# Kernel optimization log

Measured on AMD Instinct MI355X. Metric: run time of the kernel, lower is better.

Reference implementation:

```python
import jax, jax.numpy as jnp
import numpy as np

N = 100000   # nodes
E = 400000   # edges
G = 5000     # graphs (20 nodes each)
H = 128      # hidden_channels
ATOM_D, BOND_D, BOOL_D = 16, 8, 2
NODE_D = 30 + ATOM_D + 3 * BOOL_D   # 52
EDGE_D = 2 + BOND_D + 3 * BOOL_D    # 16


def setup_inputs() -> dict:
    key = jax.random.key(0)
    ks = jax.random.split(key, 24)
    rn = lambda k, shape: jax.random.normal(k, shape, dtype=jnp.float32) * 0.05
    # node features: [atom_idx, 10 continuous, 3 bools]
    atom_idx = jax.random.randint(ks[0], (N,), 1, 119)
    node_cont = jax.random.normal(ks[1], (N, 10), dtype=jnp.float32)
    node_bool = jax.random.randint(ks[2], (N, 3), 0, 2)
    x = jnp.concatenate([atom_idx[:, None].astype(jnp.float32), node_cont,
                         node_bool.astype(jnp.float32)], axis=1)
    # edge features: [bond_idx, 1 continuous, 3 bools]
    bond_idx = jax.random.randint(ks[3], (E,), 1, 22)
    edge_cont = jax.random.normal(ks[4], (E, 1), dtype=jnp.float32)
    edge_bool = jax.random.randint(ks[5], (E, 3), 0, 2)
    edge_attr = jnp.concatenate([bond_idx[:, None].astype(jnp.float32), edge_cont,
                                 edge_bool.astype(jnp.float32)], axis=1)
    edge_index = jax.random.randint(ks[6], (2, E), 0, N)
    batch = jnp.repeat(jnp.arange(G, dtype=jnp.int32), N // G)
    # embeddings (with padding rows zeroed, as nn.Embedding padding_idx)
    atom_emb = rn(ks[7], (119, ATOM_D)).at[0].set(0.0)
    bond_emb = rn(ks[8], (22, BOND_D)).at[0].set(0.0)
    bool_emb = rn(ks[9], (3, BOOL_D)).at[2].set(0.0)
    Wn = rn(ks[10], (10, 30)); bn = jnp.zeros((30,), jnp.float32)
    We = rn(ks[11], (1, 2));   be = jnp.zeros((2,), jnp.float32)
    Wl1 = rn(ks[12], (NODE_D, H)); bl1 = jnp.zeros((H,), jnp.float32)
    Wr1 = rn(ks[13], (NODE_D, H)); br1 = jnp.zeros((H,), jnp.float32)
    Wedge1 = rn(ks[14], (EDGE_D, H)); att1 = rn(ks[15], (H,))
    bias1 = jnp.zeros((H,), jnp.float32)
    Wl2 = rn(ks[16], (H, H)); bl2 = jnp.zeros((H,), jnp.float32)
    Wr2 = rn(ks[17], (H, H)); br2 = jnp.zeros((H,), jnp.float32)
    Wedge2 = rn(ks[18], (EDGE_D, H)); att2 = rn(ks[19], (H,))
    bias2 = jnp.zeros((H,), jnp.float32)
    return dict(x=x, edge_index=edge_index, edge_attr=edge_attr, batch=batch,
                atom_emb=atom_emb, bond_emb=bond_emb, bool_emb=bool_emb,
                Wn=Wn, bn=bn, We=We, be=be,
                Wl1=Wl1, bl1=bl1, Wr1=Wr1, br1=br1, Wedge1=Wedge1, att1=att1, bias1=bias1,
                Wl2=Wl2, bl2=bl2, Wr2=Wr2, br2=br2, Wedge2=Wedge2, att2=att2, bias2=bias2)


def _gatv2(h, src, dst, e_lin, Wl, bl, Wr, br, att, bias):
    # PyG GATv2Conv, heads=1: xl = lin_l(x) (source), xr = lin_r(x) (target)
    xl = h @ Wl + bl
    xr = h @ Wr + br
    m = xl[src] + xr[dst] + e_lin                      # [E', H]
    a = jax.nn.leaky_relu(m, 0.2) @ att                # [E']
    amax = jax.ops.segment_max(a, dst, num_segments=N)
    ex = jnp.exp(a - amax[dst])
    denom = jax.ops.segment_sum(ex, dst, num_segments=N)
    alpha = ex / denom[dst]                            # softmax over incoming edges
    out = jax.ops.segment_sum(alpha[:, None] * xl[src], dst, num_segments=N)
    return out + bias


def reference(x, edge_index, edge_attr, batch,
              atom_emb, bond_emb, bool_emb, Wn, bn, We, be,
              Wl1, bl1, Wr1, br1, Wedge1, att1, bias1,
              Wl2, bl2, Wr2, br2, Wedge2, att2, bias2):
    # --- encode nodes ---
    ai = x[:, 0].astype(jnp.int32)
    nb = x[:, 11:14].astype(jnp.int32)
    h = jnp.concatenate([atom_emb[ai], x[:, 1:11] @ Wn + bn,
                         bool_emb[nb[:, 0]], bool_emb[nb[:, 1]], bool_emb[nb[:, 2]]], axis=1)
    # --- encode edges ---
    bi = edge_attr[:, 0].astype(jnp.int32)
    eb = edge_attr[:, 2:5].astype(jnp.int32)
    e = jnp.concatenate([bond_emb[bi], edge_attr[:, 1:2] @ We + be,
                         bool_emb[eb[:, 0]], bool_emb[eb[:, 1]], bool_emb[eb[:, 2]]], axis=1)
    src, dst = edge_index[0], edge_index[1]
    # --- add self loops with fill_value='mean' (mean of in-edge attrs per node) ---
    cnt = jax.ops.segment_sum(jnp.ones((E,), h.dtype), dst, num_segments=N)
    loop_attr = jax.ops.segment_sum(e, dst, num_segments=N) / jnp.maximum(cnt, 1.0)[:, None]
    e_full = jnp.concatenate([e, loop_attr], axis=0)          # [E+N, EDGE_D]
    loop = jnp.arange(N, dtype=src.dtype)
    src_f = jnp.concatenate([src, loop])
    dst_f = jnp.concatenate([dst, loop])
    # --- 3 GATv2 layers (layers 2 and 3 share weights, as in the original) ---
    h = jax.nn.relu(_gatv2(h, src_f, dst_f, e_full @ Wedge1, Wl1, bl1, Wr1, br1, att1, bias1))
    e_lin2 = e_full @ Wedge2
    h = jax.nn.relu(_gatv2(h, src_f, dst_f, e_lin2, Wl2, bl2, Wr2, br2, att2, bias2))
    h = jax.nn.relu(_gatv2(h, src_f, dst_f, e_lin2, Wl2, bl2, Wr2, br2, att2, bias2))
    # --- global_max_pool readout ---
    return jax.ops.segment_max(h, batch, num_segments=G)
```

## Files before the change

### kernel.cpp

```cpp
#include <hip/hip_runtime.h>
#include <hip/hip_fp16.h>

#define N_NODES 100000
#define N_EDGES 400000
#define N_GRAPHS 5000
#define NPG 20
#define SCAN_NB 256
#define SCAN_CHUNK ((N_NODES + SCAN_NB - 1) / SCAN_NB)
#define TAB_STRIDE (256 * 128 + 128)
#define F1 8192
#define F2 16384
#define NB_ENC ((N_NODES + 255) / 256)
#define NB_HIST ((N_EDGES + 255) / 256)

typedef __attribute__((ext_vector_type(8))) _Float16 f16x8;
typedef __attribute__((ext_vector_type(2))) _Float16 h2;
typedef __attribute__((ext_vector_type(4))) float f32x4;

#define DPP_QUAD_XOR1 0xB1
#define DPP_QUAD_XOR2 0x4E
#define DPP_ROW_HALF_MIRROR 0x141
#define DPP_ROW_MIRROR 0x140
template <int CTRL>
__device__ __forceinline__ float dpp_add(float x) {
  int p = __builtin_amdgcn_update_dpp(0, __float_as_int(x), CTRL, 0xf, 0xf, true);
  return x + __int_as_float(p);
}

__global__ __launch_bounds__(256) void k_prologue(
    const float* __restrict__ x, const float* __restrict__ atom_emb,
    const float* __restrict__ bool_emb, const float* __restrict__ Wn,
    const float* __restrict__ bn, __half* __restrict__ h0,
    const int* __restrict__ dst, int* __restrict__ cnt,
    const float* __restrict__ Wedge1, const float* __restrict__ Wedge2,
    const float* __restrict__ bond_emb, const float* __restrict__ We,
    const float* __restrict__ be, __half* __restrict__ tabs,
    const float* __restrict__ Wl1, const float* __restrict__ Wr1,
    const float* __restrict__ Wl2, const float* __restrict__ Wr2,
    unsigned short* __restrict__ fr) {
  int b = blockIdx.x, tid = threadIdx.x;
  if (b < NB_ENC) {
    int n = b * 256 + tid;
    if (n >= N_NODES) return;
    const float* xr = x + (size_t)n * 14;
    int ai = (int)xr[0];
    _Float16 hr[64];
    #pragma unroll
    for (int j = 0; j < 16; j++) hr[j] = (_Float16)atom_emb[ai * 16 + j];
    float xc[10];
    #pragma unroll
    for (int k = 0; k < 10; k++) xc[k] = xr[1 + k];
    #pragma unroll
    for (int c = 0; c < 30; c++) {
      float s = bn[c];
      #pragma unroll
      for (int k = 0; k < 10; k++) s += xc[k] * Wn[k * 30 + c];
      hr[16 + c] = (_Float16)s;
    }
    #pragma unroll
    for (int t = 0; t < 3; t++) {
      int bb = (int)xr[11 + t];
      hr[46 + 2 * t]     = (_Float16)bool_emb[2 * bb];
      hr[46 + 2 * t + 1] = (_Float16)bool_emb[2 * bb + 1];
    }
    #pragma unroll
    for (int j = 52; j < 64; j++) hr[j] = (_Float16)0.0f;
    uint4* d4 = (uint4*)(h0 + (size_t)n * 64);
    const uint4* s4 = (const uint4*)hr;
    #pragma unroll
    for (int j = 0; j < 8; j++) d4[j] = s4[j];
  } else if (b < NB_ENC + NB_HIST) {
    int e = (b - NB_ENC) * 256 + tid;
    if (e >= N_EDGES) return;
    atomicAdd(cnt + dst[e], 1);
  } else if (b == NB_ENC + NB_HIST) {
    int s = tid >> 7, c = tid & 127;
    const float* W = s ? Wedge2 : Wedge1;
    __half* T12 = tabs + (size_t)s * TAB_STRIDE;
    __half* v   = T12 + 256 * 128;
    float w8 = W[8 * 128 + c], w9 = W[9 * 128 + c];
    v[c] = __float2half(We[0] * w8 + We[1] * w9);
    float cst = be[0] * w8 + be[1] * w9;
    float bond[22];
    for (int bb = 0; bb < 22; bb++) {
      float acc = 0.f;
      #pragma unroll
      for (int k = 0; k < 8; k++) acc += bond_emb[bb * 8 + k] * W[k * 128 + c];
      bond[bb] = acc;
    }
    for (int combo = 0; combo < 8; combo++) {
      float t2 = cst;
      #pragma unroll
      for (int tt = 0; tt < 3; tt++) {
        int bt = (combo >> tt) & 1;
        t2 += bool_emb[bt * 2 + 0] * W[(10 + 2 * tt + 0) * 128 + c];
        t2 += bool_emb[bt * 2 + 1] * W[(10 + 2 * tt + 1) * 128 + c];
      }
      for (int bb = 0; bb < 22; bb++)
        T12[(combo * 32 + bb) * 128 + c] = __float2half(bond[bb] + t2);
      for (int bb = 22; bb < 32; bb++)
        T12[(combo * 32 + bb) * 128 + c] = __float2half(0.f);
    }
  } else {
    int g = (b - (NB_ENC + NB_HIST + 1)) * 256 + tid;
    const float* W; int K; unsigned short* base; int fl;
    if (g < 1024)      { W = Wl1; K = 52;  base = fr;               fl = g; }
    else if (g < 2048) { W = Wr1; K = 52;  base = fr + F1;          fl = g - 1024; }
    else if (g < 4096) { W = Wl2; K = 128; base = fr + 2 * F1;      fl = g - 2048; }
    else if (g < 6144) { W = Wr2; K = 128; base = fr + 2 * F1 + F2; fl = g - 4096; }
    else return;
    int l = fl & 63, ctn = fl >> 6;
    int tn = ctn & 7, c = ctn >> 3;
    int n = tn * 16 + (l & 15);
    int kb = c * 32 + (l >> 4) * 8;
    unsigned h8[8];
    #pragma unroll
    for (int j = 0; j < 8; j++) {
      int k = kb + j;
      float v = (k < K) ? W[(size_t)k * 128 + n] : 0.f;
      __half hv = __float2half(v);
      h8[j] = (unsigned)*(unsigned short*)&hv;
    }
    uint4 hv4 = make_uint4(h8[0] | (h8[1] << 16), h8[2] | (h8[3] << 16),
                           h8[4] | (h8[5] << 16), h8[6] | (h8[7] << 16));
    *(uint4*)(base + (size_t)fl * 8) = hv4;
  }
}

__global__ __launch_bounds__(256) void k_scan1(const int* __restrict__ cnt,
                                               int* __restrict__ bsum,
                                               int* __restrict__ ghist) {
  __shared__ int red[256];
  __shared__ int lh[64];
  int b = blockIdx.x, t = threadIdx.x;
  if (t < 64) lh[t] = 0;
  __syncthreads();
  int beg = b * SCAN_CHUNK;
  int end = beg + SCAN_CHUNK; if (end > N_NODES) end = N_NODES;
  int s = 0;
  for (int i = beg + t; i < end; i += 256) {
    int cv = cnt[i];
    s += cv + 1;
    atomicAdd(&lh[cv < 63 ? cv : 63], 1);
  }
  red[t] = s;
  __syncthreads();
  for (int off = 128; off > 0; off >>= 1) {
    if (t < off) red[t] += red[t + off];
    __syncthreads();
  }
  if (t == 0) bsum[b] = red[0];
  if (t < 64 && lh[t] > 0) atomicAdd(&ghist[t], lh[t]);
}

__global__ __launch_bounds__(256) void k_scan3(const int* __restrict__ cnt,
                                               const int* __restrict__ bsum,
                                               int* __restrict__ indptr,
                                               int* __restrict__ cursor,
                                               const int* __restrict__ ghist,
                                               int* __restrict__ gcur) {
  __shared__ int sh[256];
  __shared__ int carry;
  int b = blockIdx.x, t = threadIdx.x;
  sh[t] = bsum[t];
  __syncthreads();
  for (int off = 1; off < 256; off <<= 1) {
    int v = (t >= off) ? sh[t - off] : 0;
    __syncthreads();
    sh[t] += v;
    __syncthreads();
  }
  if (t == 0) carry = (b > 0) ? sh[b - 1] : 0;
  __syncthreads();
  int beg = b * SCAN_CHUNK;
  int end = beg + SCAN_CHUNK; if (end > N_NODES) end = N_NODES;
  for (int base = beg; base < end; base += 256) {
    int i = base + t;
    int v = (i < end) ? cnt[i] + 1 : 0;
    sh[t] = v;
    __syncthreads();
    for (int off = 1; off < 256; off <<= 1) {
      int u = (t >= off) ? sh[t - off] : 0;
      __syncthreads();
      sh[t] += u;
      __syncthreads();
    }
    int excl = sh[t] - v;
    if (i < end) {
      int val = carry + excl;
      indptr[i] = val;
      cursor[i] = val;
    }
    __syncthreads();
    if (t == 255) carry += sh[255];
    __syncthreads();
  }
  if (b == 0 && t == 0) indptr[N_NODES] = N_EDGES + N_NODES;
  if (b == 0) {
    __syncthreads();
    if (t < 64) sh[t] = ghist[t];
    __syncthreads();
    if (t == 0) {
      int run = 0;
      for (int i = 0; i < 64; i++) { int v = sh[i]; sh[i] = run; run += v; }
    }
    __syncthreads();
    if (t < 64) gcur[t] = sh[t];
  }
}

__global__ void k_fill(const int* __restrict__ srcA,
                       const int* __restrict__ dst,
                       const float* __restrict__ eattr,
                       int* __restrict__ cursor,
                       int4* __restrict__ scode,
                       const int* __restrict__ cnt,
                       int* __restrict__ gcur,
                       int* __restrict__ perm) {
  int b = blockIdx.x, t = threadIdx.x;
  if (b < NB_HIST) {
    int e = b * 256 + t;
    if (e >= N_EDGES) return;
    const float* r = eattr + (size_t)e * 5;
    int bi = (int)r[0];
    float ec = r[1];
    int combo = (int)r[2] + 2 * (int)r[3] + 4 * (int)r[4];
    int meta = bi | (combo << 5);
    int d = dst[e];
    int p = atomicAdd(&cursor[d], 1);
    scode[p] = make_int4(srcA[e], meta, __float_as_int(ec), 0);
  } else {
    __shared__ int lh[64];
    __shared__ int lbase[64];
    if (t < 64) lh[t] = 0;
    __syncthreads();
    int n = (b - NB_HIST) * 256 + t;
    bool v = (n < N_NODES);
    int dc = 0, r = 0;
    if (v) {
      int cv = cnt[n];
      dc = cv < 63 ? cv : 63;
      r = atomicAdd(&lh[dc], 1);
    }
    __syncthreads();
    if (t < 64 && lh[t] > 0) lbase[t] = atomicAdd(&gcur[t], lh[t]);
    __syncthreads();
    if (v) perm[lbase[dc] + r] = n;
  }
}

template <int KPAD>
__global__ __launch_bounds__(256, 4) void k_gemm2m(const __half* __restrict__ A,
                                                   const unsigned short* __restrict__ WfL,
                                                   const unsigned short* __restrict__ WfR,
                                                   const float* __restrict__ bl_,
                                                   const float* __restrict__ br_,
                                                   __half* __restrict__ outl,
                                                   __half* __restrict__ outr) {
  __shared__ unsigned short Bs[2][8192];
  const int tid = threadIdx.x;
  const int wv = tid >> 6, lane = tid & 63;
  const int tw = blockIdx.x * 4 + wv;
  const bool active = (tw < N_NODES / 16);
  const int ml = lane & 15, q = lane >> 4;
  const int m0 = active ? tw * 16 : 0;
  f32x4 accL[8], accR[8];
  #pragma unroll
  for (int t = 0; t < 8; t++) {
    accL[t] = (f32x4){0.f, 0.f, 0.f, 0.f};
    accR[t] = (f32x4){0.f, 0.f, 0.f, 0.f};
  }
  const _Float16* ar0 = (const _Float16*)A + (size_t)(m0 + ml) * KPAD + q * 8;
  constexpr int NC2 = KPAD / 64;
  for (int c2 = 0; c2 < NC2; c2++) {
    #pragma unroll
    for (int i0 = 0; i0 < 1024; i0 += 256) {
      int i = i0 + tid;
      size_t g = ((size_t)c2 * 1024 + i) * 8;
      *(uint4*)(&Bs[0][i * 8]) = *(const uint4*)(WfL + g);
      *(uint4*)(&Bs[1][i * 8]) = *(const uint4*)(WfR + g);
    }
    __syncthreads();
    #pragma unroll
    for (int sub = 0; sub < 2; sub++) {
      f16x8 a = *(const f16x8*)(ar0 + c2 * 64 + sub * 32);
      #pragma unroll
      for (int t = 0; t < 8; t++) {
        int idx = (sub * 512 + t * 64 + lane) * 8;
        f16x8 bL = *(const f16x8*)(&Bs[0][idx]);
        f16x8 bR = *(const f16x8*)(&Bs[1][idx]);
        accL[t] = __builtin_amdgcn_mfma_f32_16x16x32_f16(a, bL, accL[t], 0, 0, 0);
        accR[t] = __builtin_amdgcn_mfma_f32_16x16x32_f16(a, bR, accR[t], 0, 0, 0);
      }
    }
    __syncthreads();
  }
  __syncthreads();
  if (!active) return;
  __half* eb = (__half*)&Bs[0][0] + wv * 2048;
  const int srow = q * 4;
  const int rrow0 = lane >> 4;
  const int rcol = (lane & 15) * 8;
  #pragma unroll
  for (int t = 0; t < 8; t++) {
    int n = t * 16 + ml;
    float bL = bl_[n];
    #pragma unroll
    for (int r = 0; r < 4; r++)
      eb[(srow + r) * 128 + n] = __float2half(accL[t][r] + bL);
  }
  #pragma unroll
  for (int pp = 0; pp < 4; pp++) {
    uint4 v = *(const uint4*)(eb + pp * 512 + lane * 8);
    *(uint4*)(outl + (size_t)(m0 + pp * 4 + rrow0) * 128 + rcol) = v;
  }
  #pragma unroll
  for (int t = 0; t < 8; t++) {
    int n = t * 16 + ml;
    float bR = br_[n];
    #pragma unroll
    for (int r = 0; r < 4; r++)
      eb[(srow + r) * 128 + n] = __float2half(accR[t][r] + bR);
  }
  #pragma unroll
  for (int pp = 0; pp < 4; pp++) {
    uint4 v = *(const uint4*)(eb + pp * 512 + lane * 8);
    *(uint4*)(outr + (size_t)(m0 + pp * 4 + rrow0) * 128 + rcol) = v;
  }
}

__global__ __launch_bounds__(256) void k_gat(const __half* __restrict__ xl,
                                             const __half* __restrict__ xr,
                                             const int* __restrict__ indptr,
                                             const int4* __restrict__ scode,
                                             const __half* __restrict__ tabs,
                                             const float* __restrict__ att,
                                             const float* __restrict__ bias,
                                             __half* __restrict__ hout,
                                             const int* __restrict__ perm) {
  int wid = (blockIdx.x * 256 + threadIdx.x) >> 6;
  int nw = (gridDim.x * 256) >> 6;
  int lane = threadIdx.x & 63;
  int q4 = lane >> 4;
  int c = (lane & 15) * 8;
  const __half* T12 = tabs;
  uint4 vu = *(const uint4*)(tabs + 256 * 128 + c);
  h2 v4[4] = {*reinterpret_cast<h2*>(&vu.x), *reinterpret_cast<h2*>(&vu.y),
              *reinterpret_cast<h2*>(&vu.z), *reinterpret_cast<h2*>(&vu.w)};
  float4 af0 = *(const float4*)(att + c);
  float4 af1 = *(const float4*)(att + c + 4);
  h2 a4[4] = {{(_Float16)af0.x, (_Float16)af0.y}, {(_Float16)af0.z, (_Float16)af0.w},
              {(_Float16)af1.x, (_Float16)af1.y}, {(_Float16)af1.z, (_Float16)af1.w}};
  float bb[8];
  {
    float4 b0 = *(const float4*)(bias + c);
    float4 b1 = *(const float4*)(bias + c + 4);
    bb[0] = b0.x; bb[1] = b0.y; bb[2] = b0.z; bb[3] = b0.w;
    bb[4] = b1.x; bb[5] = b1.y; bb[6] = b1.z; bb[7] = b1.w;
  }
  const h2 z2 = {(_Float16)0.f, (_Float16)0.f};
  const h2 k2 = {(_Float16)0.2f, (_Float16)0.2f};
  wid = __builtin_amdgcn_readfirstlane(wid);
  const int stride = nw * 4;
  int nb = wid * 4;
  if (nb >= N_NODES) return;
  int n = perm[nb + q4];
  int bg = indptr[n], en = indptr[n + 1];
  uint4 xru = *(const uint4*)(xr + (size_t)n * 128 + c);
  while (true) {
    int nb2 = nb + stride;
    bool has2 = (nb2 < N_NODES);
    int n2 = has2 ? perm[nb2 + q4] : n;
    int bg2 = indptr[n2];
    int en2 = indptr[n2 + 1];
    uint4 xru2 = *(const uint4*)(xr + (size_t)n2 * 128 + c);
    int beg = bg, end1 = en - 1;
    int last = (end1 > beg) ? end1 - 1 : beg;
    h2 xrv[4] = {*reinterpret_cast<h2*>(&xru.x), *reinterpret_cast<h2*>(&xru.y),
                 *reinterpret_cast<h2*>(&xru.z), *reinterpret_cast<h2*>(&xru.w)};
    float denom = 0.f;
    float acc[8] = {0.f, 0.f, 0.f, 0.f, 0.f, 0.f, 0.f, 0.f};
    h2 els[4] = {z2, z2, z2, z2};
    int my_it = (end1 - beg + 3) >> 2;
    int m1 = my_it, m2;
    m2 = __shfl_xor(m1, 16, 64); m1 = m1 > m2 ? m1 : m2;
    m2 = __shfl_xor(m1, 32, 64); m1 = m1 > m2 ? m1 : m2;
    int iters = m1;
    for (int it = 0; it < iters; it++) {
      int j = beg + it * 4;
      int4 sc4[4]; h2 xlv[4][4]; float tt[4];
      bool val[4];
      #pragma unroll
      for (int u = 0; u < 4; u++) {
        val[u] = (j + u < end1);
        int jj = val[u] ? j + u : last;
        sc4[u] = scode[jj];
      }
      #pragma unroll
      for (int u = 0; u < 4; u++) {
        int s = val[u] ? sc4[u].x : n;
        uint4 lv = *(const uint4*)(xl + (size_t)s * 128 + c);
        xlv[u][0] = *reinterpret_cast<h2*>(&lv.x);
        xlv[u][1] = *reinterpret_cast<h2*>(&lv.y);
        xlv[u][2] = *reinterpret_cast<h2*>(&lv.z);
        xlv[u][3] = *reinterpret_cast<h2*>(&lv.w);
      }
      #pragma unroll
      for (int u = 0; u < 4; u++) {
        int meta = val[u] ? (sc4[u].y & 255) : 255;
        float ec = val[u] ? __int_as_float(sc4[u].z) : 0.f;
        uint4 tv = *(const uint4*)(T12 + (size_t)meta * 128 + c);
        h2 t4[4] = {*reinterpret_cast<h2*>(&tv.x), *reinterpret_cast<h2*>(&tv.y),
                    *reinterpret_cast<h2*>(&tv.z), *reinterpret_cast<h2*>(&tv.w)};
        _Float16 eh = (_Float16)ec;
        h2 eh2 = {eh, eh};
        h2 d = z2;
        #pragma unroll
        for (int k = 0; k < 4; k++) {
          h2 el = eh2 * v4[k] + t4[k];
          h2 m = xlv[u][k] + xrv[k] + el;
          h2 l = __builtin_elementwise_max(m, z2) + k2 * __builtin_elementwise_min(m, z2);
          d += l * a4[k];
          els[k] += el;
        }
        tt[u] = (float)d[0] + (float)d[1];
      }
      #pragma unroll
      for (int u = 0; u < 4; u++) tt[u] = dpp_add<DPP_QUAD_XOR1>(tt[u]);
      #pragma unroll
      for (int u = 0; u < 4; u++) tt[u] = dpp_add<DPP_QUAD_XOR2>(tt[u]);
      #pragma unroll
      for (int u = 0; u < 4; u++) tt[u] = dpp_add<DPP_ROW_HALF_MIRROR>(tt[u]);
      #pragma unroll
      for (int u = 0; u < 4; u++) tt[u] = dpp_add<DPP_ROW_MIRROR>(tt[u]);
      #pragma unroll
      for (int u = 0; u < 4; u++) {
        float ex = val[u] ? __expf(tt[u]) : 0.f;
        denom += ex;
        #pragma unroll
        for (int k = 0; k < 4; k++) {
          acc[2 * k]     += ex * (float)xlv[u][k][0];
          acc[2 * k + 1] += ex * (float)xlv[u][k][1];
        }
      }
    }
    int cntn = end1 - beg;
    float inv_cnt = 1.0f / (float)(cntn > 0 ? cntn : 1);
    uint4 xnu = *(const uint4*)(xl + (size_t)n * 128 + c);
    h2 xn[4] = {*reinterpret_cast<h2*>(&xnu.x), *reinterpret_cast<h2*>(&xnu.y),
                *reinterpret_cast<h2*>(&xnu.z), *reinterpret_cast<h2*>(&xnu.w)};
    float afv[8] = {af0.x, af0.y, af0.z, af0.w, af1.x, af1.y, af1.z, af1.w};
    float ts = 0.f;
    float xnf[8];
    #pragma unroll
    for (int k = 0; k < 4; k++) {
      #pragma unroll
      for (int hh = 0; hh < 2; hh++) {
        int i = 2 * k + hh;
        xnf[i] = (float)xn[k][hh];
        float m = xnf[i] + (float)xrv[k][hh] + (float)els[k][hh] * inv_cnt;
        float l = m > 0.f ? m : 0.2f * m;
        ts += l * afv[i];
      }
    }
    ts = dpp_add<DPP_QUAD_XOR1>(ts);
    ts = dpp_add<DPP_QUAD_XOR2>(ts);
    ts = dpp_add<DPP_ROW_HALF_MIRROR>(ts);
    ts = dpp_add<DPP_ROW_MIRROR>(ts);
    float ex = __expf(ts);
    denom += ex;
    #pragma unroll
    for (int i = 0; i < 8; i++) acc[i] += ex * xnf[i];
    float invd = 1.0f / denom;
    h2 p[4];
    #pragma unroll
    for (int k = 0; k < 4; k++) {
      float o0 = acc[2 * k] * invd + bb[2 * k];
      float o1 = acc[2 * k + 1] * invd + bb[2 * k + 1];
      o0 = o0 > 0.f ? o0 : 0.f;
      o1 = o1 > 0.f ? o1 : 0.f;
      p[k] = (h2){(_Float16)o0, (_Float16)o1};
    }
    uint4 st = make_uint4(*reinterpret_cast<unsigned*>(&p[0]),
                          *reinterpret_cast<unsigned*>(&p[1]),
                          *reinterpret_cast<unsigned*>(&p[2]),
                          *reinterpret_cast<unsigned*>(&p[3]));
    *(uint4*)(hout + (size_t)n * 128 + c) = st;
    if (!has2) break;
    nb = nb2; n = n2; bg = bg2; en = en2; xru = xru2;
  }
}

__global__ void k_readout(const __half* __restrict__ h, float* __restrict__ out) {
  int wid = (blockIdx.x * blockDim.x + threadIdx.x) >> 6;
  int lane = threadIdx.x & 63;
  if (wid >= N_GRAPHS) return;
  int c = lane * 2;
  float m0 = -1e30f, m1 = -1e30f;
  for (int i = 0; i < NPG; i++) {
    unsigned v = *(const unsigned*)(h + ((size_t)(wid * NPG + i)) * 128 + c);
    h2 f = *reinterpret_cast<h2*>(&v);
    m0 = fmaxf(m0, (float)f[0]);
    m1 = fmaxf(m1, (float)f[1]);
  }
  float2 o; o.x = m0; o.y = m1;
  *(float2*)(out + (size_t)wid * 128 + c) = o;
}

extern "C" void kernel_launch(void* const* d_in, const int* in_sizes, int n_in,
                              void* d_out, int out_size, void* d_ws, size_t ws_size,
                              hipStream_t stream) {
  (void)in_sizes; (void)n_in; (void)out_size; (void)ws_size;
  const float* x        = (const float*)d_in[0];
  const int*   eindex   = (const int*)d_in[1];
  const float* eattr    = (const float*)d_in[2];
  const float* atom_emb = (const float*)d_in[4];
  const float* bond_emb = (const float*)d_in[5];
  const float* bool_emb = (const float*)d_in[6];
  const float* Wn   = (const float*)d_in[7];
  const float* bn   = (const float*)d_in[8];
  const float* We   = (const float*)d_in[9];
  const float* be   = (const float*)d_in[10];
  const float* Wl1  = (const float*)d_in[11];
  const float* bl1  = (const float*)d_in[12];
  const float* Wr1  = (const float*)d_in[13];
  const float* br1  = (const float*)d_in[14];
  const float* Wedge1 = (const float*)d_in[15];
  const float* att1 = (const float*)d_in[16];
  const float* bias1 = (const float*)d_in[17];
  const float* Wl2  = (const float*)d_in[18];
  const float* bl2  = (const float*)d_in[19];
  const float* Wr2  = (const float*)d_in[20];
  const float* br2  = (const float*)d_in[21];
  const float* Wedge2 = (const float*)d_in[22];
  const float* att2 = (const float*)d_in[23];
  const float* bias2 = (const float*)d_in[24];

  const int* srcA = eindex;
  const int* dstA = eindex + N_EDGES;

  char* p = (char*)d_ws;
  auto alloc = [&](size_t bytes) {
    char* r = p;
    p += (bytes + 255) & ~(size_t)255;
    return r;
  };
  __half* h0     = (__half*)alloc((size_t)N_NODES * 64 * 2);
  __half* h      = (__half*)alloc((size_t)N_NODES * 128 * 2);
  __half* xl     = (__half*)alloc((size_t)N_NODES * 128 * 2);
  __half* xrb    = (__half*)alloc((size_t)N_NODES * 128 * 2);
  int*    cnt    = (int*)alloc((size_t)N_NODES * 4);
  int*    indptr = (int*)alloc((size_t)(N_NODES + 1) * 4);
  int*    cursor = (int*)alloc((size_t)N_NODES * 4);
  int4*   scode  = (int4*)alloc((size_t)(N_EDGES + N_NODES) * 16);
  __half* tabs   = (__half*)alloc((size_t)2 * TAB_STRIDE * 2);
  unsigned short* wfrag = (unsigned short*)alloc((size_t)(2 * F1 + 2 * F2) * 2);
  int*    bsum   = (int*)alloc((size_t)SCAN_NB * 4);
  int*    ghist  = (int*)alloc((size_t)64 * 4);
  int*    gcur   = (int*)alloc((size_t)64 * 4);
  int*    perm   = (int*)alloc((size_t)N_NODES * 4);

  (void)hipMemsetAsync(cnt, 0, (size_t)N_NODES * 4, stream);
  (void)hipMemsetAsync(ghist, 0, (size_t)64 * 4, stream);

  k_prologue<<<NB_ENC + NB_HIST + 1 + 24, 256, 0, stream>>>(
      x, atom_emb, bool_emb, Wn, bn, h0, dstA, cnt,
      Wedge1, Wedge2, bond_emb, We, be, tabs,
      Wl1, Wr1, Wl2, Wr2, wfrag);
  k_scan1<<<SCAN_NB, 256, 0, stream>>>(cnt, bsum, ghist);
  k_scan3<<<SCAN_NB, 256, 0, stream>>>(cnt, bsum, indptr, cursor, ghist, gcur);
  k_fill<<<NB_HIST + NB_ENC, 256, 0, stream>>>(srcA, dstA, eattr, cursor, scode,
                                               cnt, gcur, perm);

  const unsigned short* f_l1 = wfrag;
  const unsigned short* f_r1 = wfrag + F1;
  const unsigned short* f_l2 = wfrag + 2 * F1;
  const unsigned short* f_r2 = wfrag + 2 * F1 + F2;

  const int GB2 = (N_NODES / 16 + 3) / 4;

  k_gemm2m<64><<<GB2, 256, 0, stream>>>(h0, f_l1, f_r1, bl1, br1, xl, xrb);
  k_gat<<<2048, 256, 0, stream>>>(xl, xrb, indptr, scode, tabs, att1, bias1, h, perm);

  k_gemm2m<128><<<GB2, 256, 0, stream>>>(h, f_l2, f_r2, bl2, br2, xl, xrb);
  k_gat<<<2048, 256, 0, stream>>>(xl, xrb, indptr, scode, tabs + TAB_STRIDE, att2, bias2, h, perm);

  k_gemm2m<128><<<GB2, 256, 0, stream>>>(h, f_l2, f_r2, bl2, br2, xl, xrb);
  k_gat<<<2048, 256, 0, stream>>>(xl, xrb, indptr, scode, tabs + TAB_STRIDE, att2, bias2, h, perm);

  k_readout<<<(N_GRAPHS * 64 + 255) / 256, 256, 0, stream>>>(h, (float*)d_out);
}
```

Baseline: 334.6 us.

## Software-pipeline GAT edge loop with double-buffered gathers and prefetched edge codes

Restructures the per-node edge aggregation loop in the GAT kernel into a two-stage software pipeline. Edge codes are loaded two iterations ahead, and the xl-row and table gathers for the next iteration are issued before the current iteration's compute, using A/B register buffers. The goal is to hide global-memory gather latency behind the attention math. The extra buffers raise VGPR pressure and may lower occupancy.

```diff
diff --git a/kernel.cpp b/kernel.cpp
--- a/kernel.cpp
+++ b/kernel.cpp
@@ -344,9 +344,9 @@
   int q4 = lane >> 4;
   int c = (lane & 15) * 8;
   const __half* T12 = tabs;
-  uint4 vu = *(const uint4*)(tabs + 256 * 128 + c);
-  h2 v4[4] = {*reinterpret_cast<h2*>(&vu.x), *reinterpret_cast<h2*>(&vu.y),
-              *reinterpret_cast<h2*>(&vu.z), *reinterpret_cast<h2*>(&vu.w)};
+  uint4 vu_ = *(const uint4*)(tabs + 256 * 128 + c);
+  h2 v4[4] = {*reinterpret_cast<h2*>(&vu_.x), *reinterpret_cast<h2*>(&vu_.y),
+              *reinterpret_cast<h2*>(&vu_.z), *reinterpret_cast<h2*>(&vu_.w)};
   float4 af0 = *(const float4*)(att + c);
   float4 af1 = *(const float4*)(att + c + 4);
   h2 a4[4] = {{(_Float16)af0.x, (_Float16)af0.y}, {(_Float16)af0.z, (_Float16)af0.w},
@@ -386,33 +386,42 @@
     m2 = __shfl_xor(m1, 16, 64); m1 = m1 > m2 ? m1 : m2;
     m2 = __shfl_xor(m1, 32, 64); m1 = m1 > m2 ? m1 : m2;
     int iters = m1;
-    for (int it = 0; it < iters; it++) {
-      int j = beg + it * 4;
-      int4 sc4[4]; h2 xlv[4][4]; float tt[4];
-      bool val[4];
+
+    auto LOADSC = [&](int4* sc, int it_) {
+      int j = beg + it_ * 4;
       #pragma unroll
       for (int u = 0; u < 4; u++) {
-        val[u] = (j + u < end1);
-        int jj = val[u] ? j + u : last;
-        sc4[u] = scode[jj];
-      }
+        int jj = (j + u < end1) ? j + u : last;
+        sc[u] = scode[jj];
+      }
+    };
+    auto ISSUE = [&](uint4* lv, uint4* tv, float* ec, const int4* sc, int it_) {
+      int j = beg + it_ * 4;
       #pragma unroll
       for (int u = 0; u < 4; u++) {
-        int s = val[u] ? sc4[u].x : n;
-        uint4 lv = *(const uint4*)(xl + (size_t)s * 128 + c);
-        xlv[u][0] = *reinterpret_cast<h2*>(&lv.x);
-        xlv[u][1] = *reinterpret_cast<h2*>(&lv.y);
-        xlv[u][2] = *reinterpret_cast<h2*>(&lv.z);
-        xlv[u][3] = *reinterpret_cast<h2*>(&lv.w);
-      }
+        bool vu = (j + u < end1);
+        int s = vu ? sc[u].x : n;
+        lv[u] = *(const uint4*)(xl + (size_t)s * 128 + c);
+        int meta = vu ? (sc[u].y & 255) : 255;
+        tv[u] = *(const uint4*)(T12 + (size_t)meta * 128 + c);
+        ec[u] = vu ? __int_as_float(sc[u].z) : 0.f;
+      }
+    };
+    auto COMPUTE = [&](const uint4* lv, const uint4* tv, const float* ec, int it_) {
+      int j = beg + it_ * 4;
+      float tt[4];
+      h2 xlv[4][4];
       #pragma unroll
       for (int u = 0; u < 4; u++) {
-        int meta = val[u] ? (sc4[u].y & 255) : 255;
-        float ec = val[u] ? __int_as_float(sc4[u].z) : 0.f;
-        uint4 tv = *(const uint4*)(T12 + (size_t)meta * 128 + c);
-        h2 t4[4] = {*reinterpret_cast<h2*>(&tv.x), *reinterpret_cast<h2*>(&tv.y),
-                    *reinterpret_cast<h2*>(&tv.z), *reinterpret_cast<h2*>(&tv.w)};
-        _Float16 eh = (_Float16)ec;
+        xlv[u][0] = *reinterpret_cast<const h2*>(&lv[u].x);
+        xlv[u][1] = *reinterpret_cast<const h2*>(&lv[u].y);
+        xlv[u][2] = *reinterpret_cast<const h2*>(&lv[u].z);
+        xlv[u][3] = *reinterpret_cast<const h2*>(&lv[u].w);
+        h2 t4[4] = {*reinterpret_cast<const h2*>(&tv[u].x),
+                    *reinterpret_cast<const h2*>(&tv[u].y),
+                    *reinterpret_cast<const h2*>(&tv[u].z),
+                    *reinterpret_cast<const h2*>(&tv[u].w)};
+        _Float16 eh = (_Float16)ec[u];
         h2 eh2 = {eh, eh};
         h2 d = z2;
         #pragma unroll
@@ -435,13 +444,41 @@
       for (int u = 0; u < 4; u++) tt[u] = dpp_add<DPP_ROW_MIRROR>(tt[u]);
       #pragma unroll
       for (int u = 0; u < 4; u++) {
-        float ex = val[u] ? __expf(tt[u]) : 0.f;
+        bool vu = (j + u < end1);
+        float ex = vu ? __expf(tt[u]) : 0.f;
         denom += ex;
         #pragma unroll
         for (int k = 0; k < 4; k++) {
           acc[2 * k]     += ex * (float)xlv[u][k][0];
           acc[2 * k + 1] += ex * (float)xlv[u][k][1];
         }
+      }
+    };
+
+    if (iters > 0) {
+      int4 scN[4];
+      uint4 lvA[4], tvA[4]; float ecA[4];
+      uint4 lvB[4], tvB[4]; float ecB[4];
+      {
+        int4 sc0[4];
+        LOADSC(sc0, 0);
+        ISSUE(lvA, tvA, ecA, sc0, 0);
+        if (iters > 1) LOADSC(scN, 1);
+      }
+      for (int it = 0; it < iters; ) {
+        if (it + 1 < iters) {
+          ISSUE(lvB, tvB, ecB, scN, it + 1);
+          if (it + 2 < iters) LOADSC(scN, it + 2);
+        }
+        COMPUTE(lvA, tvA, ecA, it);
+        it++;
+        if (it >= iters) break;
+        if (it + 1 < iters) {
+          ISSUE(lvA, tvA, ecA, scN, it + 1);
+          if (it + 2 < iters) LOADSC(scN, it + 2);
+        }
+        COMPUTE(lvB, tvB, ecB, it);
+        it++;
       }
     }
     int cntn = end1 - beg;
```

New measurement: 346.4 us. 1.04x slower.
